# Performance work log

Measured on AMD Instinct MI355X. Metric: run time of the kernel, lower is better.

Reference implementation:

```python
import jax, jax.numpy as jnp
import numpy as np

N = 100000      # nodes
E = 1600000     # edges
IN = 128        # in_channels
ED = 32         # edge_dim
H = 4           # heads
C = 32          # out_channels per head
NEG_SLOPE = 0.2


def setup_inputs() -> dict:
    key = jax.random.key(0)
    ks = jax.random.split(key, 10)
    s = 0.1  # glorot-ish scale
    return {
        "x": jax.random.normal(ks[0], (N, IN), dtype=jnp.float32),
        "edge_index": jax.random.randint(ks[1], (2, E), 0, N, dtype=jnp.int32),
        "edge_attr": jax.random.normal(ks[2], (E, ED), dtype=jnp.float32),
        "W": jax.random.normal(ks[3], (IN, H * C), dtype=jnp.float32) * s,
        "att_src": jax.random.normal(ks[4], (H, C), dtype=jnp.float32) * s,
        "att_dst": jax.random.normal(ks[5], (H, C), dtype=jnp.float32) * s,
        "W_edge": jax.random.normal(ks[6], (ED, H * C), dtype=jnp.float32) * s,
        "att_edge": jax.random.normal(ks[7], (H, C), dtype=jnp.float32) * s,
        "gat_bias": jnp.zeros((H * C,), dtype=jnp.float32),
        "bias": jnp.zeros((C,), dtype=jnp.float32),
    }


def reference(x, edge_index, edge_attr, W, att_src, att_dst, W_edge, att_edge, gat_bias, bias):
    # eval mode: no dropout. GATConv with edge_dim, concat=True, then mean over heads.
    src, dst = edge_index[0], edge_index[1]
    xh = (x @ W).reshape(N, H, C)                       # [N,H,C]
    a_src = jnp.einsum("nhc,hc->nh", xh, att_src)      # [N,H]
    a_dst = jnp.einsum("nhc,hc->nh", xh, att_dst)      # [N,H]
    eh = (edge_attr @ W_edge).reshape(E, H, C)          # [E,H,C]
    a_edge = jnp.einsum("ehc,hc->eh", eh, att_edge)    # [E,H]
    logits = a_src[src] + a_dst[dst] + a_edge           # [E,H]
    logits = jnp.where(logits >= 0, logits, NEG_SLOPE * logits)  # leaky_relu
    # segment softmax over edges grouped by destination node
    seg_max = jax.ops.segment_max(logits, dst, num_segments=N)  # [N,H]
    expv = jnp.exp(logits - seg_max[dst])
    denom = jax.ops.segment_sum(expv, dst, num_segments=N)      # [N,H]
    alpha = expv / denom[dst]                                    # [E,H]
    msg = xh[src] * alpha[:, :, None]                            # [E,H,C]
    out = jax.ops.segment_sum(msg, dst, num_segments=N)          # [N,H,C]
    out = out + gat_bias.reshape(1, H, C)                        # GATConv bias (concat)
    out = out.mean(axis=1)                                       # combine='mean' -> [N,C]
    out = out + bias
    return jax.nn.relu(out)
```

## Files before the change

kernel.cpp:

```cpp
#include <hip/hip_runtime.h>
#include <hip/hip_bf16.h>

typedef __hip_bfloat16 bf16;

#define N_NODES 100000
#define N_EDGES 1600000
#define IN_CH   128
#define ED_DIM  32
#define HEADS   4
#define C_OUT   32
#define HC      128
#define NEG_SLOPE 0.2f
#define SCAN_BLOCKS 98
#define PREP_BLOCKS 392
#define NG_BLOCKS 3125

__device__ __forceinline__ float bf_lo(unsigned u) { return __uint_as_float(u << 16); }
__device__ __forceinline__ float bf_hi(unsigned u) { return __uint_as_float(u & 0xffff0000u); }
__device__ __forceinline__ unsigned short f2bf_rne(float f) {
    unsigned u = __float_as_uint(f);
    return (unsigned short)((u + 0x7fffu + ((u >> 16) & 1u)) >> 16);
}
__device__ __forceinline__ unsigned pack_bf2(float a, float b) {
    return ((unsigned)f2bf_rne(b) << 16) | f2bf_rne(a);
}
__device__ __forceinline__ float load_any(const void* p, int i, int isf32) {
    return isf32 ? ((const float*)p)[i]
                 : __uint_as_float(((unsigned)((const unsigned short*)p)[i]) << 16);
}

__global__ void report_err(unsigned short* out, float code) {
    if (threadIdx.x < 16) out[threadIdx.x] = f2bf_rne(code);
}

__global__ __launch_bounds__(256) void prep_small(
    const void* __restrict__ x,
    const void* __restrict__ W, const void* __restrict__ att_src,
    const void* __restrict__ att_dst, const void* __restrict__ W_edge,
    const void* __restrict__ att_edge, const void* __restrict__ gat_bias,
    const void* __restrict__ bias,
    int* __restrict__ flag,
    unsigned short* __restrict__ Wc, float* __restrict__ att_src_f,
    float* __restrict__ att_dst_f, float* __restrict__ gat_bias_f,
    float* __restrict__ bias_f, float* __restrict__ Wa,
    int* __restrict__ count) {

    int t = threadIdx.x;
    int gi = blockIdx.x * 256 + t;
    if (gi < N_NODES) count[gi] = 0;
    if (blockIdx.x != 0) return;

    __shared__ int cnt;
    if (t == 0) cnt = 0;
    __syncthreads();
    unsigned xw = ((const unsigned*)x)[t];
    int ex = (xw >> 7) & 0xFF;
    if (ex >= 140) atomicAdd(&cnt, 1);
    __syncthreads();
    int isf32 = (cnt >= 32) ? 1 : 0;
    if (t == 0) *flag = isf32;

    for (int i = t; i < IN_CH * HC; i += 256)
        Wc[i] = f2bf_rne(load_any(W, i, isf32));
    if (t < 128) {
        att_src_f[t]  = load_any(att_src, t, isf32);
        att_dst_f[t]  = load_any(att_dst, t, isf32);
        gat_bias_f[t] = load_any(gat_bias, t, isf32);
    }
    if (t < 32) bias_f[t] = load_any(bias, t, isf32);
    if (t < 128) {
        int d = t & 31, h = t >> 5;
        float acc = 0.f;
        for (int c = 0; c < C_OUT; ++c)
            acc += load_any(W_edge, d * HC + h * C_OUT + c, isf32) *
                   load_any(att_edge, h * C_OUT + c, isf32);
        Wa[h * 32 + d] = acc;
    }
}

__global__ __launch_bounds__(256) void node_gemm(
    const int* __restrict__ flag, const void* __restrict__ x,
    const int* __restrict__ ei,
    const unsigned short* __restrict__ Wc,
    const float* __restrict__ att_src_f, const float* __restrict__ att_dst_f,
    unsigned short* __restrict__ xh,
    float* __restrict__ a_src, float* __restrict__ a_dst,
    int* __restrict__ count, int* __restrict__ rank) {

    __shared__ unsigned short Wl[IN_CH * HC];
    __shared__ float xl[32 * IN_CH];

    int isf32 = *flag;
    int t = threadIdx.x;
    int node0 = blockIdx.x * 32;

    {
        int p = blockIdx.x * 256 + t;
        const uint2* dst2 = (const uint2*)(ei + N_EDGES);
        uint2 d2 = dst2[p];
        int r0 = atomicAdd(&count[d2.x], 1);
        int r1 = atomicAdd(&count[d2.y], 1);
        ((int2*)rank)[p] = make_int2(r0, r1);
    }

    const uint4* Wg = (const uint4*)Wc;
    uint4* Wl4 = (uint4*)Wl;
#pragma unroll
    for (int k = 0; k < 8; ++k) Wl4[t + k * 256] = Wg[t + k * 256];

    if (isf32) {
        const float4* xg = (const float4*)((const float*)x + (size_t)node0 * IN_CH);
        float4* xl4 = (float4*)xl;
#pragma unroll
        for (int k = 0; k < 4; ++k) xl4[t + k * 256] = xg[t + k * 256];
    } else {
        const unsigned* xg = (const unsigned*)((const unsigned short*)x + (size_t)node0 * IN_CH);
#pragma unroll
        for (int k = 0; k < 8; ++k) {
            unsigned u = xg[t + k * 256];
            int f = 2 * (t + k * 256);
            xl[f]     = bf_lo(u);
            xl[f + 1] = bf_hi(u);
        }
    }
    __syncthreads();

    int q  = t & 31;
    int i0 = (t >> 5) * 4;
    int j4 = q * 4;
    float acc[16];
#pragma unroll
    for (int k = 0; k < 16; ++k) acc[k] = 0.f;

    const float* xr0 = xl + (i0 + 0) * IN_CH;
    const float* xr1 = xl + (i0 + 1) * IN_CH;
    const float* xr2 = xl + (i0 + 2) * IN_CH;
    const float* xr3 = xl + (i0 + 3) * IN_CH;

#pragma unroll 8
    for (int d = 0; d < IN_CH; ++d) {
        uint2 wb = *(const uint2*)(Wl + d * HC + j4);
        float w0 = bf_lo(wb.x), w1 = bf_hi(wb.x);
        float w2 = bf_lo(wb.y), w3 = bf_hi(wb.y);
        float x0 = xr0[d], x1 = xr1[d], x2 = xr2[d], x3 = xr3[d];
        acc[0]  += x0 * w0; acc[1]  += x0 * w1; acc[2]  += x0 * w2; acc[3]  += x0 * w3;
        acc[4]  += x1 * w0; acc[5]  += x1 * w1; acc[6]  += x1 * w2; acc[7]  += x1 * w3;
        acc[8]  += x2 * w0; acc[9]  += x2 * w1; acc[10] += x2 * w2; acc[11] += x2 * w3;
        acc[12] += x3 * w0; acc[13] += x3 * w1; acc[14] += x3 * w2; acc[15] += x3 * w3;
    }

    float4 sa = *(const float4*)(att_src_f + j4);
    float4 da = *(const float4*)(att_dst_f + j4);

#pragma unroll
    for (int k = 0; k < 4; ++k) {
        int node = node0 + i0 + k;
        float a0 = acc[4 * k], a1 = acc[4 * k + 1], a2 = acc[4 * k + 2], a3 = acc[4 * k + 3];
        *(uint2*)(xh + (size_t)node * HC + j4) =
            make_uint2(pack_bf2(a0, a1), pack_bf2(a2, a3));

        float ps = a0 * sa.x + a1 * sa.y + a2 * sa.z + a3 * sa.w;
        float pd = a0 * da.x + a1 * da.y + a2 * da.z + a3 * da.w;
        ps += __shfl_xor(ps, 1); ps += __shfl_xor(ps, 2); ps += __shfl_xor(ps, 4);
        pd += __shfl_xor(pd, 1); pd += __shfl_xor(pd, 2); pd += __shfl_xor(pd, 4);
        if ((q & 7) == 0) {
            int h = q >> 3;
            a_src[node * HEADS + h] = ps;
            a_dst[node * HEADS + h] = pd;
        }
    }
}

__global__ __launch_bounds__(256) void scan_a(const int* __restrict__ count,
                                              int* __restrict__ starts,
                                              int* __restrict__ blockSums) {
    __shared__ int sd[256];
    int t = threadIdx.x;
    int base = blockIdx.x * 1024 + t * 4;
    int c0 = (base + 0 < N_NODES) ? count[base + 0] : 0;
    int c1 = (base + 1 < N_NODES) ? count[base + 1] : 0;
    int c2 = (base + 2 < N_NODES) ? count[base + 2] : 0;
    int c3 = (base + 3 < N_NODES) ? count[base + 3] : 0;
    int s = c0 + c1 + c2 + c3;
    sd[t] = s;
    __syncthreads();
    for (int off = 1; off < 256; off <<= 1) {
        int v = (t >= off) ? sd[t - off] : 0;
        __syncthreads();
        sd[t] += v;
        __syncthreads();
    }
    int excl = sd[t] - s;
    if (base + 0 < N_NODES) starts[base + 0] = excl;
    if (base + 1 < N_NODES) starts[base + 1] = excl + c0;
    if (base + 2 < N_NODES) starts[base + 2] = excl + c0 + c1;
    if (base + 3 < N_NODES) starts[base + 3] = excl + c0 + c1 + c2;
    if (t == 255) blockSums[blockIdx.x] = sd[255];
}

__global__ __launch_bounds__(128) void scan_b(int* __restrict__ blockSums) {
    __shared__ int sd[128];
    int t = threadIdx.x;
    int v = (t < SCAN_BLOCKS) ? blockSums[t] : 0;
    sd[t] = v;
    __syncthreads();
    for (int off = 1; off < 128; off <<= 1) {
        int u = (t >= off) ? sd[t - off] : 0;
        __syncthreads();
        sd[t] += u;
        __syncthreads();
    }
    if (t < SCAN_BLOCKS) blockSums[t] = sd[t] - v;
}

__global__ __launch_bounds__(256) void scan_c(int* __restrict__ starts,
                                              const int* __restrict__ blockSums) {
    int off = blockSums[blockIdx.x];
    int base = blockIdx.x * 1024 + threadIdx.x * 4;
#pragma unroll
    for (int k = 0; k < 4; ++k) {
        int idx = base + k;
        if (idx < N_NODES) starts[idx] += off;
    }
    if (blockIdx.x == 0 && threadIdx.x == 0) starts[N_NODES] = N_EDGES;
}

__global__ __launch_bounds__(256) void edge_scatter(
    const int* __restrict__ flag,
    const int* __restrict__ ei, const void* __restrict__ edge_attr,
    const float* __restrict__ a_src, const float* __restrict__ a_dst,
    const float* __restrict__ Wa,
    const int* __restrict__ starts, const int* __restrict__ rank,
    uint4* __restrict__ perm4) {

    __shared__ float WaL[128];
    int t = threadIdx.x;
    if (t < 128) WaL[t] = Wa[t];
    __syncthreads();

    int isf32 = *flag;
    int e = blockIdx.x * 256 + t;
    if (e >= N_EDGES) return;
    int s  = ei[e];
    int dn = ei[N_EDGES + e];
    int pos = starts[dn] + rank[e];

    float ae0 = 0.f, ae1 = 0.f, ae2 = 0.f, ae3 = 0.f;
    if (isf32) {
        const float4* ea = (const float4*)((const float*)edge_attr + (size_t)e * ED_DIM);
#pragma unroll
        for (int k = 0; k < 8; ++k) {
            float4 v = ea[k];
            int d = 4 * k;
            ae0 += v.x * WaL[d] + v.y * WaL[d + 1] + v.z * WaL[d + 2] + v.w * WaL[d + 3];
            ae1 += v.x * WaL[32 + d] + v.y * WaL[33 + d] + v.z * WaL[34 + d] + v.w * WaL[35 + d];
            ae2 += v.x * WaL[64 + d] + v.y * WaL[65 + d] + v.z * WaL[66 + d] + v.w * WaL[67 + d];
            ae3 += v.x * WaL[96 + d] + v.y * WaL[97 + d] + v.z * WaL[98 + d] + v.w * WaL[99 + d];
        }
    } else {
        const uint4* ea = (const uint4*)((const unsigned short*)edge_attr + (size_t)e * ED_DIM);
#pragma unroll
        for (int k = 0; k < 4; ++k) {
            uint4 v = ea[k];
            float g0 = bf_lo(v.x), g1 = bf_hi(v.x), g2 = bf_lo(v.y), g3 = bf_hi(v.y);
            float g4 = bf_lo(v.z), g5 = bf_hi(v.z), g6 = bf_lo(v.w), g7 = bf_hi(v.w);
            int d = 8 * k;
            ae0 += g0*WaL[d] + g1*WaL[d+1] + g2*WaL[d+2] + g3*WaL[d+3]
                 + g4*WaL[d+4] + g5*WaL[d+5] + g6*WaL[d+6] + g7*WaL[d+7];
            ae1 += g0*WaL[32+d] + g1*WaL[33+d] + g2*WaL[34+d] + g3*WaL[35+d]
                 + g4*WaL[36+d] + g5*WaL[37+d] + g6*WaL[38+d] + g7*WaL[39+d];
            ae2 += g0*WaL[64+d] + g1*WaL[65+d] + g2*WaL[66+d] + g3*WaL[67+d]
                 + g4*WaL[68+d] + g5*WaL[69+d] + g6*WaL[70+d] + g7*WaL[71+d];
            ae3 += g0*WaL[96+d] + g1*WaL[97+d] + g2*WaL[98+d] + g3*WaL[99+d]
                 + g4*WaL[100+d] + g5*WaL[101+d] + g6*WaL[102+d] + g7*WaL[103+d];
        }
    }

    float4 as = *(const float4*)(a_src + (size_t)s * 4);
    float4 ad = *(const float4*)(a_dst + (size_t)dn * 4);
    float l0 = as.x + ad.x + ae0;
    float l1 = as.y + ad.y + ae1;
    float l2 = as.z + ad.z + ae2;
    float l3 = as.w + ad.w + ae3;
    l0 = (l0 >= 0.f) ? l0 : NEG_SLOPE * l0;
    l1 = (l1 >= 0.f) ? l1 : NEG_SLOPE * l1;
    l2 = (l2 >= 0.f) ? l2 : NEG_SLOPE * l2;
    l3 = (l3 >= 0.f) ? l3 : NEG_SLOPE * l3;
    float w0 = __expf(l0), w1 = __expf(l1), w2 = __expf(l2), w3 = __expf(l3);

    perm4[pos] = make_uint4((unsigned)s, pack_bf2(w0, w1), pack_bf2(w2, w3), 0u);
}

__global__ __launch_bounds__(256) void gather(
    const int* __restrict__ flag,
    const int* __restrict__ starts, const uint4* __restrict__ perm4,
    const unsigned short* __restrict__ xh,
    const float* __restrict__ gat_bias_f, const float* __restrict__ bias_f,
    void* __restrict__ out) {

    __shared__ uint4 sR[4][64];

    int t = threadIdx.x;
    int w = t >> 6, lane = t & 63;
    int quarter = lane >> 4;
    int l = lane & 15;
    int h = l >> 2;
    int n = blockIdx.x * 4 + w;
    if (n >= N_NODES) return;
    int isf32 = *flag;

    int st = starts[n], en = starts[n + 1];
    float f0 = 0.f, f1 = 0.f, f2 = 0.f, f3 = 0.f;
    float f4 = 0.f, f5 = 0.f, f6 = 0.f, f7 = 0.f, wsum = 0.f;

    for (int base = st; base < en; base += 64) {
        int cnt = en - base;
        if (cnt > 64) cnt = 64;
        __builtin_amdgcn_wave_barrier();
        if (lane < cnt) sR[w][lane] = perm4[base + lane];
        __builtin_amdgcn_wave_barrier();
#pragma unroll 4
        for (int jj = 0; jj < cnt; jj += 4) {
            int j = jj + quarter;
            int valid = (j < cnt);
            int jc = valid ? j : jj;
            uint4 r = sR[w][jc];
            int s = (int)r.x;
            unsigned hw = (h & 2) ? r.z : r.y;
            float wt = (h & 1) ? bf_hi(hw) : bf_lo(hw);
            wt = valid ? wt : 0.f;
            uint4 xv = *(const uint4*)(xh + ((size_t)s << 7) + 8 * l);
            f0 += wt * bf_lo(xv.x);
            f1 += wt * bf_hi(xv.x);
            f2 += wt * bf_lo(xv.y);
            f3 += wt * bf_hi(xv.y);
            f4 += wt * bf_lo(xv.z);
            f5 += wt * bf_hi(xv.z);
            f6 += wt * bf_lo(xv.w);
            f7 += wt * bf_hi(xv.w);
            wsum += wt;
        }
    }

    f0 += __shfl_xor(f0, 16); f0 += __shfl_xor(f0, 32);
    f1 += __shfl_xor(f1, 16); f1 += __shfl_xor(f1, 32);
    f2 += __shfl_xor(f2, 16); f2 += __shfl_xor(f2, 32);
    f3 += __shfl_xor(f3, 16); f3 += __shfl_xor(f3, 32);
    f4 += __shfl_xor(f4, 16); f4 += __shfl_xor(f4, 32);
    f5 += __shfl_xor(f5, 16); f5 += __shfl_xor(f5, 32);
    f6 += __shfl_xor(f6, 16); f6 += __shfl_xor(f6, 32);
    f7 += __shfl_xor(f7, 16); f7 += __shfl_xor(f7, 32);
    wsum += __shfl_xor(wsum, 16); wsum += __shfl_xor(wsum, 32);

    float inv = (wsum > 0.f) ? 1.f / wsum : 0.f;
    int cg = 8 * l;
    float v0 = f0 * inv + gat_bias_f[cg];
    float v1 = f1 * inv + gat_bias_f[cg + 1];
    float v2 = f2 * inv + gat_bias_f[cg + 2];
    float v3 = f3 * inv + gat_bias_f[cg + 3];
    float v4 = f4 * inv + gat_bias_f[cg + 4];
    float v5 = f5 * inv + gat_bias_f[cg + 5];
    float v6 = f6 * inv + gat_bias_f[cg + 6];
    float v7 = f7 * inv + gat_bias_f[cg + 7];
    v0 += __shfl_xor(v0, 4); v0 += __shfl_xor(v0, 8);
    v1 += __shfl_xor(v1, 4); v1 += __shfl_xor(v1, 8);
    v2 += __shfl_xor(v2, 4); v2 += __shfl_xor(v2, 8);
    v3 += __shfl_xor(v3, 4); v3 += __shfl_xor(v3, 8);
    v4 += __shfl_xor(v4, 4); v4 += __shfl_xor(v4, 8);
    v5 += __shfl_xor(v5, 4); v5 += __shfl_xor(v5, 8);
    v6 += __shfl_xor(v6, 4); v6 += __shfl_xor(v6, 8);
    v7 += __shfl_xor(v7, 4); v7 += __shfl_xor(v7, 8);

    if (lane < 4) {
        int c = 8 * lane;
        float o0 = fmaxf(v0 * 0.25f + bias_f[c],     0.f);
        float o1 = fmaxf(v1 * 0.25f + bias_f[c + 1], 0.f);
        float o2 = fmaxf(v2 * 0.25f + bias_f[c + 2], 0.f);
        float o3 = fmaxf(v3 * 0.25f + bias_f[c + 3], 0.f);
        float o4 = fmaxf(v4 * 0.25f + bias_f[c + 4], 0.f);
        float o5 = fmaxf(v5 * 0.25f + bias_f[c + 5], 0.f);
        float o6 = fmaxf(v6 * 0.25f + bias_f[c + 6], 0.f);
        float o7 = fmaxf(v7 * 0.25f + bias_f[c + 7], 0.f);
        if (isf32) {
            float* op = (float*)out + (size_t)n * C_OUT + c;
            *(float4*)(op)     = make_float4(o0, o1, o2, o3);
            *(float4*)(op + 4) = make_float4(o4, o5, o6, o7);
        } else {
            unsigned p0 = ((unsigned)f2bf_rne(o1) << 16) | f2bf_rne(o0);
            unsigned p1 = ((unsigned)f2bf_rne(o3) << 16) | f2bf_rne(o2);
            unsigned p2 = ((unsigned)f2bf_rne(o5) << 16) | f2bf_rne(o4);
            unsigned p3 = ((unsigned)f2bf_rne(o7) << 16) | f2bf_rne(o6);
            *(uint4*)((unsigned short*)out + (size_t)n * C_OUT + c) =
                make_uint4(p0, p1, p2, p3);
        }
    }
}

extern "C" void kernel_launch(void* const* d_in, const int* in_sizes, int n_in,
                              void* d_out, int out_size, void* d_ws, size_t ws_size,
                              hipStream_t stream) {
    const void* x         = d_in[0];
    const int*  ei        = (const int*)d_in[1];
    const void* edge_attr = d_in[2];
    const void* W         = d_in[3];
    const void* att_src   = d_in[4];
    const void* att_dst   = d_in[5];
    const void* W_edge    = d_in[6];
    const void* att_edge  = d_in[7];
    const void* gat_bias  = d_in[8];
    const void* bias      = d_in[9];

    char* ws = (char*)d_ws;
    size_t off = 0;
    auto align256 = [](size_t v) { return (v + 255) & ~(size_t)255; };

    unsigned short* xh = (unsigned short*)(ws + off);
    off = align256(off + (size_t)N_NODES * HC * sizeof(unsigned short));
    float* a_src_w = (float*)(ws + off);
    off = align256(off + (size_t)N_NODES * HEADS * sizeof(float));
    float* a_dst_w = (float*)(ws + off);
    off = align256(off + (size_t)N_NODES * HEADS * sizeof(float));
    int* count = (int*)(ws + off);
    off = align256(off + (size_t)N_NODES * sizeof(int));
    int* starts = (int*)(ws + off);
    off = align256(off + (size_t)(N_NODES + 1) * sizeof(int));
    int* rank = (int*)(ws + off);
    off = align256(off + (size_t)N_EDGES * sizeof(int));
    int* blockSums = (int*)(ws + off);
    off = align256(off + (size_t)SCAN_BLOCKS * sizeof(int));
    uint4* perm4 = (uint4*)(ws + off);
    off = align256(off + (size_t)N_EDGES * sizeof(uint4));
    float* Wa = (float*)(ws + off);
    off = align256(off + 128 * sizeof(float));
    unsigned short* Wc = (unsigned short*)(ws + off);
    off = align256(off + (size_t)IN_CH * HC * sizeof(unsigned short));
    float* att_src_f = (float*)(ws + off);
    off = align256(off + 128 * sizeof(float));
    float* att_dst_f = (float*)(ws + off);
    off = align256(off + 128 * sizeof(float));
    float* gat_bias_f = (float*)(ws + off);
    off = align256(off + 128 * sizeof(float));
    float* bias_f = (float*)(ws + off);
    off = align256(off + 32 * sizeof(float));
    int* dflag = (int*)(ws + off);
    off = align256(off + sizeof(int));
    size_t need = off;

    if (ws_size < need) {
        report_err<<<1, 64, 0, stream>>>((unsigned short*)d_out, 1500.0f);
        return;
    }

    (void)hipGetLastError();

    prep_small<<<PREP_BLOCKS, 256, 0, stream>>>(x, W, att_src, att_dst,
                                                W_edge, att_edge, gat_bias, bias,
                                                dflag, Wc, att_src_f, att_dst_f,
                                                gat_bias_f, bias_f, Wa, count);
    node_gemm<<<NG_BLOCKS, 256, 0, stream>>>(dflag, x, ei, Wc, att_src_f,
                                             att_dst_f, xh, a_src_w, a_dst_w,
                                             count, rank);
    scan_a<<<SCAN_BLOCKS, 256, 0, stream>>>(count, starts, blockSums);
    scan_b<<<1, 128, 0, stream>>>(blockSums);
    scan_c<<<SCAN_BLOCKS, 256, 0, stream>>>(starts, blockSums);
    edge_scatter<<<(N_EDGES + 255) / 256, 256, 0, stream>>>(dflag, ei, edge_attr,
                                                            a_src_w, a_dst_w, Wa,
                                                            starts, rank, perm4);
    gather<<<N_NODES / 4, 256, 0, stream>>>(dflag, starts, perm4,
                                            xh, gat_bias_f, bias_f, d_out);

    hipError_t e = hipGetLastError();
    if (e != hipSuccess) {
        report_err<<<1, 64, 0, stream>>>((unsigned short*)d_out,
                                         1000.0f + (float)(int)e);
    }
}
```

Measured before the change: 547.9 us.

## Use 16 lanes per edge in edge_scatter for coalesced edge_attr reads

edge_scatter now gives each edge 16 lanes, with 4 edges per wavefront in a grid-stride loop. Each lane loads a float2 or bf16 pair of edge_attr and computes partial head dot products, which are reduced with xor shuffles. Lane h of each group computes the logit and exp for head h, and lane 0 writes the packed record. This replaces per-thread 128-byte strided row loads with coalesced contiguous reads, at the cost of redundant index loads across lanes and shuffle overhead.

Measured after the change: 586.5 us. 1.07x slower.

```diff
diff --git a/kernel.cpp b/kernel.cpp
--- a/kernel.cpp
+++ b/kernel.cpp
@@ -14,6 +14,7 @@
 #define SCAN_BLOCKS 98
 #define PREP_BLOCKS 392
 #define NG_BLOCKS 3125
+#define ES_BLOCKS 6250
 
 __device__ __forceinline__ float bf_lo(unsigned u) { return __uint_as_float(u << 16); }
 __device__ __forceinline__ float bf_hi(unsigned u) { return __uint_as_float(u & 0xffff0000u); }
@@ -233,62 +234,64 @@
     const int* __restrict__ starts, const int* __restrict__ rank,
     uint4* __restrict__ perm4) {
 
-    __shared__ float WaL[128];
-    int t = threadIdx.x;
-    if (t < 128) WaL[t] = Wa[t];
-    __syncthreads();
-
+    int t = threadIdx.x;
+    int wv = t >> 6;
+    int lane = t & 63;
+    int g = lane >> 4;
+    int l = lane & 15;
     int isf32 = *flag;
-    int e = blockIdx.x * 256 + t;
-    if (e >= N_EDGES) return;
-    int s  = ei[e];
-    int dn = ei[N_EDGES + e];
-    int pos = starts[dn] + rank[e];
-
-    float ae0 = 0.f, ae1 = 0.f, ae2 = 0.f, ae3 = 0.f;
-    if (isf32) {
-        const float4* ea = (const float4*)((const float*)edge_attr + (size_t)e * ED_DIM);
-#pragma unroll
-        for (int k = 0; k < 8; ++k) {
-            float4 v = ea[k];
-            int d = 4 * k;
-            ae0 += v.x * WaL[d] + v.y * WaL[d + 1] + v.z * WaL[d + 2] + v.w * WaL[d + 3];
-            ae1 += v.x * WaL[32 + d] + v.y * WaL[33 + d] + v.z * WaL[34 + d] + v.w * WaL[35 + d];
-            ae2 += v.x * WaL[64 + d] + v.y * WaL[65 + d] + v.z * WaL[66 + d] + v.w * WaL[67 + d];
-            ae3 += v.x * WaL[96 + d] + v.y * WaL[97 + d] + v.z * WaL[98 + d] + v.w * WaL[99 + d];
-        }
-    } else {
-        const uint4* ea = (const uint4*)((const unsigned short*)edge_attr + (size_t)e * ED_DIM);
-#pragma unroll
-        for (int k = 0; k < 4; ++k) {
-            uint4 v = ea[k];
-            float g0 = bf_lo(v.x), g1 = bf_hi(v.x), g2 = bf_lo(v.y), g3 = bf_hi(v.y);
-            float g4 = bf_lo(v.z), g5 = bf_hi(v.z), g6 = bf_lo(v.w), g7 = bf_hi(v.w);
-            int d = 8 * k;
-            ae0 += g0*WaL[d] + g1*WaL[d+1] + g2*WaL[d+2] + g3*WaL[d+3]
-                 + g4*WaL[d+4] + g5*WaL[d+5] + g6*WaL[d+6] + g7*WaL[d+7];
-            ae1 += g0*WaL[32+d] + g1*WaL[33+d] + g2*WaL[34+d] + g3*WaL[35+d]
-                 + g4*WaL[36+d] + g5*WaL[37+d] + g6*WaL[38+d] + g7*WaL[39+d];
-            ae2 += g0*WaL[64+d] + g1*WaL[65+d] + g2*WaL[66+d] + g3*WaL[67+d]
-                 + g4*WaL[68+d] + g5*WaL[69+d] + g6*WaL[70+d] + g7*WaL[71+d];
-            ae3 += g0*WaL[96+d] + g1*WaL[97+d] + g2*WaL[98+d] + g3*WaL[99+d]
-                 + g4*WaL[100+d] + g5*WaL[101+d] + g6*WaL[102+d] + g7*WaL[103+d];
-        }
-    }
-
-    float4 as = *(const float4*)(a_src + (size_t)s * 4);
-    float4 ad = *(const float4*)(a_dst + (size_t)dn * 4);
-    float l0 = as.x + ad.x + ae0;
-    float l1 = as.y + ad.y + ae1;
-    float l2 = as.z + ad.z + ae2;
-    float l3 = as.w + ad.w + ae3;
-    l0 = (l0 >= 0.f) ? l0 : NEG_SLOPE * l0;
-    l1 = (l1 >= 0.f) ? l1 : NEG_SLOPE * l1;
-    l2 = (l2 >= 0.f) ? l2 : NEG_SLOPE * l2;
-    l3 = (l3 >= 0.f) ? l3 : NEG_SLOPE * l3;
-    float w0 = __expf(l0), w1 = __expf(l1), w2 = __expf(l2), w3 = __expf(l3);
-
-    perm4[pos] = make_uint4((unsigned)s, pack_bf2(w0, w1), pack_bf2(w2, w3), 0u);
+
+    float wa00 = Wa[0 * 32 + 2 * l], wa01 = Wa[0 * 32 + 2 * l + 1];
+    float wa10 = Wa[1 * 32 + 2 * l], wa11 = Wa[1 * 32 + 2 * l + 1];
+    float wa20 = Wa[2 * 32 + 2 * l], wa21 = Wa[2 * 32 + 2 * l + 1];
+    float wa30 = Wa[3 * 32 + 2 * l], wa31 = Wa[3 * 32 + 2 * l + 1];
+
+    const int nquads = N_EDGES / 4;
+    const int qstride = ES_BLOCKS * 4;
+    int h = l & 3;
+    int gbase = lane & 48;
+
+    for (int q = blockIdx.x * 4 + wv; q < nquads; q += qstride) {
+        int e = q * 4 + g;
+        int s  = ei[e];
+        int dn = ei[N_EDGES + e];
+        int pos = starts[dn] + rank[e];
+
+        float ea0, ea1;
+        if (isf32) {
+            float2 v = ((const float2*)edge_attr)[(size_t)e * 16 + l];
+            ea0 = v.x; ea1 = v.y;
+        } else {
+            unsigned u = ((const unsigned*)edge_attr)[(size_t)e * 16 + l];
+            ea0 = bf_lo(u); ea1 = bf_hi(u);
+        }
+
+        float p0 = ea0 * wa00 + ea1 * wa01;
+        float p1 = ea0 * wa10 + ea1 * wa11;
+        float p2 = ea0 * wa20 + ea1 * wa21;
+        float p3 = ea0 * wa30 + ea1 * wa31;
+        p0 += __shfl_xor(p0, 1); p0 += __shfl_xor(p0, 2);
+        p0 += __shfl_xor(p0, 4); p0 += __shfl_xor(p0, 8);
+        p1 += __shfl_xor(p1, 1); p1 += __shfl_xor(p1, 2);
+        p1 += __shfl_xor(p1, 4); p1 += __shfl_xor(p1, 8);
+        p2 += __shfl_xor(p2, 1); p2 += __shfl_xor(p2, 2);
+        p2 += __shfl_xor(p2, 4); p2 += __shfl_xor(p2, 8);
+        p3 += __shfl_xor(p3, 1); p3 += __shfl_xor(p3, 2);
+        p3 += __shfl_xor(p3, 4); p3 += __shfl_xor(p3, 8);
+
+        float ae = (h == 0) ? p0 : (h == 1) ? p1 : (h == 2) ? p2 : p3;
+        float lg = a_src[4 * s + h] + a_dst[4 * dn + h] + ae;
+        lg = (lg >= 0.f) ? lg : NEG_SLOPE * lg;
+        float wgt = __expf(lg);
+
+        float w1v = __shfl(wgt, gbase + 1);
+        float w2v = __shfl(wgt, gbase + 2);
+        float w3v = __shfl(wgt, gbase + 3);
+        if (l == 0) {
+            perm4[pos] = make_uint4((unsigned)s, pack_bf2(wgt, w1v),
+                                    pack_bf2(w2v, w3v), 0u);
+        }
+    }
 }
 
 __global__ __launch_bounds__(256) void gather(
@@ -463,9 +466,9 @@
     scan_a<<<SCAN_BLOCKS, 256, 0, stream>>>(count, starts, blockSums);
     scan_b<<<1, 128, 0, stream>>>(blockSums);
     scan_c<<<SCAN_BLOCKS, 256, 0, stream>>>(starts, blockSums);
-    edge_scatter<<<(N_EDGES + 255) / 256, 256, 0, stream>>>(dflag, ei, edge_attr,
-                                                            a_src_w, a_dst_w, Wa,
-                                                            starts, rank, perm4);
+    edge_scatter<<<ES_BLOCKS, 256, 0, stream>>>(dflag, ei, edge_attr,
+                                                a_src_w, a_dst_w, Wa,
+                                                starts, rank, perm4);
     gather<<<N_NODES / 4, 256, 0, stream>>>(dflag, starts, perm4,
                                             xh, gat_bias_f, bias_f, d_out);
 
```
